# Performance work log

Hardware: AMD Instinct MI355X
Metric: run time of the kernel (lower is better)

The kernel has to match this reference:

```python
import jax, jax.numpy as jnp
import numpy as np

EPS = 1e-5
NEG = -10000.0


def rel_shift(x):
    # x: [B, H, T1, T2] with T2 = 2*T1 - 1 -> returns [B, H, T1, T1]
    B, H, T1, T2 = x.shape
    x = jnp.pad(x, ((0, 0), (0, 0), (0, 0), (1, 0)))        # [B,H,T1,T2+1]
    x = x.reshape(B, H, T2 + 1, T1)[:, :, 1:, :].reshape(B, H, T1, T2)
    return x[:, :, :, : T2 // 2 + 1]


def setup_inputs() -> dict:
    key = jax.random.key(0)
    B, C, T, H = 4, 512, 1024, 8
    ks = jax.random.split(key, 16)
    s = 0.02
    inp = {
        "x": jax.random.normal(ks[0], (B, C, T), jnp.float32),
        "pos_emb": jax.random.normal(ks[1], (1, C, 2 * T - 1), jnp.float32),
        "x_mask": jnp.ones((B, 1, T), jnp.float32),
        "gamma": jnp.ones((C,), jnp.float32),
        "beta": jnp.zeros((C,), jnp.float32),
        "Wq": jax.random.normal(ks[2], (C, C), jnp.float32) * s,
        "bq": jnp.zeros((C,), jnp.float32),
        "Wk": jax.random.normal(ks[3], (C, C), jnp.float32) * s,
        "bk": jnp.zeros((C,), jnp.float32),
        "Wv": jax.random.normal(ks[4], (C, C), jnp.float32) * s,
        "bv": jnp.zeros((C,), jnp.float32),
        "Wp": jax.random.normal(ks[5], (C, C), jnp.float32) * s,
        "u_bias": jax.random.normal(ks[6], (H, C // H), jnp.float32) * s,
        "v_bias": jax.random.normal(ks[7], (H, C // H), jnp.float32) * s,
        "Wo": jax.random.normal(ks[8], (C, C), jnp.float32) * s,
        "bo": jnp.zeros((C,), jnp.float32),
    }
    return inp


def reference(x, pos_emb, x_mask, gamma, beta, Wq, bq, Wk, bk, Wv, bv, Wp,
              u_bias, v_bias, Wo, bo):
    B, C, T = x.shape
    H, Dh = u_bias.shape

    # channel LayerNorm (axis=1)
    mean = jnp.mean(x, axis=1, keepdims=True)
    var = jnp.mean((x - mean) ** 2, axis=1, keepdims=True)
    xn = (x - mean) * jax.lax.rsqrt(var + EPS)
    xn = xn * gamma[None, :, None] + beta[None, :, None]

    conv1x1 = lambda W, b, z: jnp.einsum('oc,bct->bot', W, z) + b[None, :, None]
    q = conv1x1(Wq, bq, xn).reshape(B, H, Dh, T)
    k = conv1x1(Wk, bk, xn).reshape(B, H, Dh, T)
    v = conv1x1(Wv, bv, xn).reshape(B, H, Dh, T)
    p = jnp.einsum('oc,xct->xot', Wp, pos_emb)          # [1, C, 2T-1], no bias
    p = p.reshape(p.shape[0], H, Dh, -1)[0]             # [H, Dh, 2T-1]

    content = jnp.einsum('bhdt,bhds->bhts', q + u_bias[None, :, :, None], k)
    pos = jnp.einsum('bhdt,hds->bhts', q + v_bias[None, :, :, None], p)
    pos = rel_shift(pos)                                 # [B, H, T, T]

    score = (content + pos) / jnp.sqrt(jnp.float32(C))
    attn_mask = x_mask[:, :, None, :] * x_mask[:, :, :, None]  # [B,1,T,T]
    score = jnp.where(attn_mask == 0, NEG, score)
    attn = jax.nn.softmax(score, axis=-1)

    # context[d,t] = sum_s v[d,s] * attn[s,t]
    ctx = jnp.einsum('bhds,bhst->bhdt', v, attn).reshape(B, C, T)
    return jnp.einsum('oc,bct->bot', Wo, ctx) + bo[None, :, None]
```

## Files before the change

### kernel.cpp

```cpp
#include <hip/hip_runtime.h>
#include <hip/hip_bf16.h>
#include <cmath>

typedef unsigned short u16;
typedef __bf16 bf16_t;
typedef bf16_t bf16x8 __attribute__((ext_vector_type(8)));
typedef float f32x4 __attribute__((ext_vector_type(4)));
typedef u16 u16x8 __attribute__((ext_vector_type(8)));

#define MFMA16(A,B,C) __builtin_amdgcn_mfma_f32_16x16x32_bf16(A,B,C,0,0,0)

#define CB 512
#define TT 1024
#define NH 8
#define DH 64
#define ALPHA (0.044194173824159216f * 1.4426950408889634f)
#define MASKL 14426.950408889634f

static __device__ __forceinline__ u16 f2b(float f) {
  unsigned u = __float_as_uint(f);
  unsigned r = u + 0x7FFFu + ((u >> 16) & 1u);
  return (u16)(r >> 16);
}
static __device__ __forceinline__ float b2f(u16 u) {
  return __uint_as_float(((unsigned)u) << 16);
}
static __device__ __forceinline__ bf16x8 ldb8(const u16* p) {
  return *reinterpret_cast<const bf16x8*>(p);
}

__global__ __launch_bounds__(256)
void convert5(const float* __restrict__ Wq, const float* __restrict__ Wk,
              const float* __restrict__ Wv, const float* __restrict__ Wp,
              const float* __restrict__ Wo,
              u16* __restrict__ Wstk, u16* __restrict__ WoB)
{
  int i = blockIdx.x * 256 + threadIdx.x;
  int sel = i >> 15, loc = i & 32767;
  const float* src = (sel == 0) ? Wq : (sel == 1) ? Wk : (sel == 2) ? Wv
                   : (sel == 3) ? Wp : Wo;
  const float4 a = ((const float4*)src)[loc * 2 + 0];
  const float4 b = ((const float4*)src)[loc * 2 + 1];
  u16x8 o;
  o[0] = f2b(a.x); o[1] = f2b(a.y); o[2] = f2b(a.z); o[3] = f2b(a.w);
  o[4] = f2b(b.x); o[5] = f2b(b.y); o[6] = f2b(b.z); o[7] = f2b(b.w);
  u16* dst = (sel < 4) ? (Wstk + (size_t)i * 8) : (WoB + (size_t)loc * 8);
  *(u16x8*)dst = o;
}

__global__ __launch_bounds__(256)
void transpose_pe(const float* __restrict__ pe, u16* __restrict__ posT)
{
  __shared__ float tile[64][65];
  int j0 = blockIdx.x * 64, c0 = blockIdx.y * 64;
  for (int e = threadIdx.x; e < 4096; e += 256) {
    int cc = e >> 6, jj = e & 63;
    int j = j0 + jj;
    tile[jj][cc] = (j < 2047) ? pe[(size_t)(c0 + cc) * 2047 + j] : 0.f;
  }
  __syncthreads();
  for (int e = threadIdx.x; e < 4096; e += 256) {
    int jj = e >> 6, cc = e & 63;
    posT[(size_t)(j0 + jj) * 512 + c0 + cc] = f2b(tile[jj][cc]);
  }
}

__global__ __launch_bounds__(256)
void ln_kernel(const float* __restrict__ x, const float* __restrict__ gamma,
               const float* __restrict__ beta, u16* __restrict__ xnT)
{
  __shared__ float sred[8][33], ssred[8][33];
  int tl = threadIdx.x & 31, cg = threadIdx.x >> 5;
  int t = blockIdx.x * 32 + tl;
  int b = blockIdx.y;
  const float* xb = x + (size_t)b * CB * TT + t;
  float s = 0.f, ss = 0.f;
  for (int c = cg * 64; c < cg * 64 + 64; ++c) {
    float v = xb[(size_t)c * TT];
    s += v; ss += v * v;
  }
  sred[cg][tl] = s; ssred[cg][tl] = ss;
  __syncthreads();
  float S = 0.f, SS = 0.f;
  #pragma unroll
  for (int g = 0; g < 8; ++g) { S += sred[g][tl]; SS += ssred[g][tl]; }
  float mean = S * (1.f / 512.f);
  float var = SS * (1.f / 512.f) - mean * mean;
  float rstd = rsqrtf(var + 1e-5f);
  u16* orow = xnT + ((size_t)b * TT + t) * CB;
  for (int c8 = 0; c8 < 8; ++c8) {
    int c = cg * 64 + c8 * 8;
    u16x8 o;
    #pragma unroll
    for (int j = 0; j < 8; ++j) {
      float v = xb[(size_t)(c + j) * TT];
      o[j] = f2b((v - mean) * rstd * gamma[c + j] + beta[c + j]);
    }
    *(u16x8*)(orow + c) = o;
  }
}

template<int K, int OMODE>
__global__ __launch_bounds__(256)
void gemm2(const u16* __restrict__ A, const u16* __restrict__ XT,
           long xStride, long oStride, int Nout,
           const float* __restrict__ b0, void* __restrict__ outv)
{
  const int tid = threadIdx.x, w = tid >> 6, lane = tid & 63;
  const int ln16 = lane & 15, kg = lane >> 4;
  const int wm = w & 1, wn = w >> 1;
  const int m0 = blockIdx.y * 64 + wm * 32;
  const int n0 = blockIdx.x * 128 + wn * 64;
  const int z = blockIdx.z;
  const u16* Ar = A + (size_t)(m0 + ln16) * K + kg * 8;
  const u16* Br = XT + (size_t)z * xStride + (size_t)(n0 + ln16) * K + kg * 8;
  f32x4 acc[2][4] = {};
  #pragma unroll 2
  for (int ks = 0; ks < K / 32; ++ks) {
    bf16x8 a[2], bb[4];
    #pragma unroll
    for (int mt = 0; mt < 2; ++mt) a[mt] = ldb8(Ar + (size_t)mt * 16 * K + ks * 32);
    #pragma unroll
    for (int nt = 0; nt < 4; ++nt) bb[nt] = ldb8(Br + (size_t)nt * 16 * K + ks * 32);
    #pragma unroll
    for (int mt = 0; mt < 2; ++mt)
      #pragma unroll
      for (int nt = 0; nt < 4; ++nt)
        acc[mt][nt] = MFMA16(a[mt], bb[nt], acc[mt][nt]);
  }
  float add[2][4];
  #pragma unroll
  for (int mt = 0; mt < 2; ++mt)
    #pragma unroll
    for (int jr = 0; jr < 4; ++jr)
      add[mt][jr] = b0 ? b0[m0 + mt * 16 + kg * 4 + jr] : 0.f;
  #pragma unroll
  for (int mt = 0; mt < 2; ++mt)
    #pragma unroll
    for (int nt = 0; nt < 4; ++nt) {
      const int n = n0 + nt * 16 + ln16;
      if constexpr (OMODE == 0) {
        float* out = (float*)outv;
        #pragma unroll
        for (int jr = 0; jr < 4; ++jr)
          out[(size_t)z * oStride + (size_t)(m0 + mt * 16 + kg * 4 + jr) * Nout + n] =
              acc[mt][nt][jr] + add[mt][jr];
      } else {
        const int m_low = m0 + mt * 16;
        const size_t o = (size_t)z * oStride +
                         ((size_t)(m_low >> 6) * Nout + n) * 64 + (m_low & 63) + kg * 4;
        ushort4 s4;
        s4.x = f2b(acc[mt][nt][0] + add[mt][0]);
        s4.y = f2b(acc[mt][nt][1] + add[mt][1]);
        s4.z = f2b(acc[mt][nt][2] + add[mt][2]);
        s4.w = f2b(acc[mt][nt][3] + add[mt][3]);
        *reinterpret_cast<ushort4*>((u16*)outv + o) = s4;
      }
    }
}

__global__ __launch_bounds__(256)
void proj_qkv2(const u16* __restrict__ Wstk, const u16* __restrict__ xnT,
               const float* __restrict__ bq, const float* __restrict__ ub,
               const float* __restrict__ bk, const float* __restrict__ bv,
               u16* __restrict__ quB, u16* __restrict__ kB, u16* __restrict__ vB)
{
  const int tid = threadIdx.x, w = tid >> 6, lane = tid & 63;
  const int ln16 = lane & 15, kg = lane >> 4;
  const int wm = w & 1, wn = w >> 1;
  const int my = blockIdx.y;
  const int sec = my >> 3;
  const int m0l = (my & 7) * 64 + wm * 32;
  const int n0 = blockIdx.x * 128 + wn * 64;
  const int z = blockIdx.z;
  const long XS = (long)TT * CB;
  const long QS = (long)NH * TT * DH;
  const u16* Ar = Wstk + (size_t)(sec * 512 + m0l + ln16) * 512 + kg * 8;
  const u16* Br = xnT + (size_t)z * XS + (size_t)(n0 + ln16) * 512 + kg * 8;
  f32x4 acc[2][4] = {};
  #pragma unroll 2
  for (int ks = 0; ks < 16; ++ks) {
    bf16x8 a[2], bb[4];
    #pragma unroll
    for (int mt = 0; mt < 2; ++mt) a[mt] = ldb8(Ar + (size_t)mt * 16 * 512 + ks * 32);
    #pragma unroll
    for (int nt = 0; nt < 4; ++nt) bb[nt] = ldb8(Br + (size_t)nt * 16 * 512 + ks * 32);
    #pragma unroll
    for (int mt = 0; mt < 2; ++mt)
      #pragma unroll
      for (int nt = 0; nt < 4; ++nt)
        acc[mt][nt] = MFMA16(a[mt], bb[nt], acc[mt][nt]);
  }
  const float scl = (sec == 0) ? ALPHA : 1.f;
  float add[2][4];
  #pragma unroll
  for (int mt = 0; mt < 2; ++mt)
    #pragma unroll
    for (int jr = 0; jr < 4; ++jr) {
      int m = m0l + mt * 16 + kg * 4 + jr;
      add[mt][jr] = (sec == 0) ? (bq[m] + ub[m]) : (sec == 1) ? bk[m] : bv[m];
    }
  if (sec < 2) {
    u16* dst = sec ? kB : quB;
    #pragma unroll
    for (int mt = 0; mt < 2; ++mt)
      #pragma unroll
      for (int nt = 0; nt < 4; ++nt) {
        const int n = n0 + nt * 16 + ln16;
        const int m_low = m0l + mt * 16;
        const size_t o = (size_t)z * QS +
                         ((size_t)(m_low >> 6) * TT + n) * 64 + (m_low & 63) + kg * 4;
        ushort4 s4;
        s4.x = f2b((acc[mt][nt][0] + add[mt][0]) * scl);
        s4.y = f2b((acc[mt][nt][1] + add[mt][1]) * scl);
        s4.z = f2b((acc[mt][nt][2] + add[mt][2]) * scl);
        s4.w = f2b((acc[mt][nt][3] + add[mt][3]) * scl);
        *reinterpret_cast<ushort4*>(dst + o) = s4;
      }
  } else {
    #pragma unroll
    for (int mt = 0; mt < 2; ++mt)
      #pragma unroll
      for (int nt = 0; nt < 4; ++nt) {
        const int n = n0 + nt * 16 + ln16;
        #pragma unroll
        for (int jr = 0; jr < 4; ++jr)
          vB[(size_t)z * QS + (size_t)(m0l + mt * 16 + kg * 4 + jr) * TT + n] =
              f2b(acc[mt][nt][jr] + add[mt][jr]);
      }
  }
}

__global__ __launch_bounds__(256)
void corr_kernel(const u16* __restrict__ pp, const float* __restrict__ ub,
                 const float* __restrict__ vb, float* __restrict__ corr)
{
  const int h = blockIdx.y;
  const int j = blockIdx.x * 256 + threadIdx.x;
  __shared__ float dl[64];
  if (threadIdx.x < 64)
    dl[threadIdx.x] = vb[h * 64 + threadIdx.x] - ub[h * 64 + threadIdx.x];
  __syncthreads();
  const u16* prow = pp + ((size_t)h * 2048 + j) * 64;
  float s = 0.f;
  #pragma unroll
  for (int d8 = 0; d8 < 8; ++d8) {
    union { bf16x8 v; u16 u[8]; } pu;
    pu.v = ldb8(prow + d8 * 8);
    #pragma unroll
    for (int e = 0; e < 8; ++e) s += b2f(pu.u[e]) * dl[d8 * 8 + e];
  }
  corr[h * 2048 + j] = s * ALPHA;
}

__global__ __launch_bounds__(256)
void stats_mfma(const u16* __restrict__ qu, const u16* __restrict__ kk_,
                const u16* __restrict__ pp, const float* __restrict__ corr,
                const float* __restrict__ xmask, float* __restrict__ ls)
{
  const int tid = threadIdx.x;
  const int w = tid >> 6, lane = tid & 63;
  const int ln16 = lane & 15, kg = lane >> 4;
  const int l48 = lane & 48;
  const int bid = blockIdx.x;
  const int bh = (bid & 7) + 8 * ((bid >> 3) & 3);
  const int rest = bid >> 5;
  const int qi0 = (rest & 31) * 32;
  const int part = rest >> 5;
  const int b = bh >> 3, h = bh & 7;
  const u16* quP = qu + (size_t)bh * TT * DH;
  const u16* kP  = kk_ + (size_t)bh * TT * DH;
  const u16* pP  = pp + (size_t)h * 2048 * DH;
  const float* corrP = corr + (h << 11);

  __shared__ float red[4][32];

  bf16x8 qa[2][2];
  #pragma unroll
  for (int mt = 0; mt < 2; ++mt)
    #pragma unroll
    for (int kc = 0; kc < 2; ++kc)
      qa[mt][kc] = ldb8(&quP[(size_t)(qi0 + mt * 16 + ln16) * DH + kc * 32 + kg * 8]);
  float aq[2][4];
  #pragma unroll
  for (int mt = 0; mt < 2; ++mt)
    #pragma unroll
    for (int jr = 0; jr < 4; ++jr)
      aq[mt][jr] = (xmask[b * TT + qi0 + mt * 16 + kg * 4 + jr] - 1.f) * MASKL;

  float rs[2][4] = {};
  for (int c = 0; c < 2; ++c) {
    const int ki0 = (part * 8 + c * 4 + w) * 64;
    const int j0 = ki0 - qi0 + 992;
    #pragma unroll
    for (int mt = 0; mt < 2; ++mt) {
      f32x4 g[6];
      #pragma unroll
      for (int n = 0; n < 6; ++n) {
        const size_t po = (size_t)(j0 + n * 16 + ln16) * DH + kg * 8;
        bf16x8 pb0 = ldb8(&pP[po]);
        bf16x8 pb1 = ldb8(&pP[po + 32]);
        const float cval = corrP[j0 + n * 16 + ln16];
        f32x4 t = {cval, cval, cval, cval};
        t = MFMA16(qa[mt][0], pb0, t);
        t = MFMA16(qa[mt][1], pb1, t);
        g[n] = t;
      }
      f32x4 dd[4];
      #pragma unroll
      for (int nt = 0; nt < 4; ++nt) {
        const size_t ko = (size_t)(ki0 + nt * 16 + ln16) * DH + kg * 8;
        bf16x8 kb0 = ldb8(&kP[ko]);
        bf16x8 kb1 = ldb8(&kP[ko + 32]);
        const float ak = (xmask[b * TT + ki0 + nt * 16 + ln16] - 1.f) * MASKL;
        f32x4 t = { aq[mt][0] + ak, aq[mt][1] + ak, aq[mt][2] + ak, aq[mt][3] + ak };
        t = MFMA16(qa[mt][0], kb0, t);
        t = MFMA16(qa[mt][1], kb1, t);
        dd[nt] = t;
      }
      #pragma unroll
      for (int jr = 0; jr < 4; ++jr) {
        const int qrow = mt * 16 + kg * 4 + jr;
        const int sh = ln16 + 31 - qrow;
        const int src = l48 | (sh & 15);
        const int o = sh >> 4;
        float s[6];
        #pragma unroll
        for (int n = 0; n < 6; ++n) s[n] = __shfl(g[n][jr], src);
        #pragma unroll
        for (int nt = 0; nt < 4; ++nt) {
          const float val = (o == 0) ? s[nt] : (o == 1) ? s[nt + 1] : s[nt + 2];
          rs[mt][jr] += exp2f(dd[nt][jr] + val);
        }
      }
    }
  }
  #pragma unroll
  for (int mt = 0; mt < 2; ++mt)
    #pragma unroll
    for (int jr = 0; jr < 4; ++jr) {
      float v = rs[mt][jr];
      v += __shfl_xor(v, 1); v += __shfl_xor(v, 2);
      v += __shfl_xor(v, 4); v += __shfl_xor(v, 8);
      rs[mt][jr] = v;
    }
  if (ln16 == 0) {
    #pragma unroll
    for (int mt = 0; mt < 2; ++mt)
      #pragma unroll
      for (int jr = 0; jr < 4; ++jr)
        red[w][mt * 16 + kg * 4 + jr] = rs[mt][jr];
  }
  __syncthreads();
  if (tid < 32)
    ls[(size_t)part * 32768 + (size_t)bh * TT + qi0 + tid] =
        red[0][tid] + red[1][tid] + red[2][tid] + red[3][tid];
}

__global__ __launch_bounds__(256)
void ctx_mfma(const u16* __restrict__ qu, const u16* __restrict__ kk_,
              const u16* __restrict__ vv, const u16* __restrict__ pp,
              const float* __restrict__ corr, const float* __restrict__ xmask,
              u16* __restrict__ ctx2)
{
  const int tid = threadIdx.x;
  const int w = tid >> 6, lane = tid & 63;
  const int ln16 = lane & 15, kg = lane >> 4;
  const int l48 = lane & 48;
  const int bid = blockIdx.x;
  const int bh = (bid & 7) + 8 * ((bid >> 3) & 3);
  const int rest = bid >> 5;
  const int t0 = (rest & 15) * 64;
  const int part = rest >> 4;
  const int b = bh >> 3, h = bh & 7;
  const u16* quP = qu + (size_t)bh * TT * DH;
  const u16* kP  = kk_ + (size_t)bh * TT * DH;
  const u16* vP  = vv + (size_t)bh * DH * TT;
  const u16* pP  = pp + (size_t)h * 2048 * DH;
  const float* corrP = corr + (h << 11);

  __shared__ __align__(16) u16 P[2][64][72];

  bf16x8 ka[4][2];
  #pragma unroll
  for (int nt = 0; nt < 4; ++nt)
    #pragma unroll
    for (int kc = 0; kc < 2; ++kc)
      ka[nt][kc] = ldb8(&kP[(size_t)(t0 + nt * 16 + ln16) * DH + kc * 32 + kg * 8]);
  float at4[4];
  #pragma unroll
  for (int nt = 0; nt < 4; ++nt)
    at4[nt] = (xmask[b * TT + t0 + nt * 16 + ln16] - 1.f) * MASKL;

  auto scores = [&](int qcn, int buf) {
    const int qw = qcn * 64 + w * 16;
    const int j0 = t0 - qw + 1008;
    const size_t qo = (size_t)(qw + ln16) * DH + kg * 8;
    bf16x8 qa0 = ldb8(&quP[qo]), qa1 = ldb8(&quP[qo + 32]);
    f32x4 g[5];
    #pragma unroll
    for (int n = 0; n < 5; ++n) {
      const size_t po = (size_t)(j0 + n * 16 + ln16) * DH + kg * 8;
      bf16x8 pb0 = ldb8(&pP[po]), pb1 = ldb8(&pP[po + 32]);
      const float cval = corrP[j0 + n * 16 + ln16];
      f32x4 t = {cval, cval, cval, cval};
      t = MFMA16(qa0, pb0, t);
      t = MFMA16(qa1, pb1, t);
      g[n] = t;
    }
    float sg[4][5];
    #pragma unroll
    for (int jr = 0; jr < 4; ++jr) {
      const int qrow = kg * 4 + jr;
      const int src = l48 | ((ln16 + 15 - qrow) & 15);
      #pragma unroll
      for (int n = 0; n < 5; ++n) sg[jr][n] = __shfl(g[n][jr], src);
    }
    float aqv[4];
    #pragma unroll
    for (int jr = 0; jr < 4; ++jr)
      aqv[jr] = (xmask[b * TT + qw + kg * 4 + jr] - 1.f) * MASKL;
    #pragma unroll
    for (int nt = 0; nt < 4; ++nt) {
      f32x4 dd = { aqv[0] + at4[nt], aqv[1] + at4[nt],
                   aqv[2] + at4[nt], aqv[3] + at4[nt] };
      dd = MFMA16(qa0, ka[nt][0], dd);
      dd = MFMA16(qa1, ka[nt][1], dd);
      unsigned lo = 0, hi = 0;
      #pragma unroll
      for (int jr = 0; jr < 4; ++jr) {
        const int qrow = kg * 4 + jr;
        const float val = (ln16 <= qrow) ? sg[jr][nt] : sg[jr][nt + 1];
        const float e = exp2f(dd[jr] + val);
        const unsigned bb = f2b(e);
        if (jr == 0) lo = bb; else if (jr == 1) lo |= bb << 16;
        else if (jr == 2) hi = bb; else hi |= bb << 16;
      }
      *reinterpret_cast<uint2*>(&P[buf][nt * 16 + ln16][w * 16 + kg * 4]) =
          make_uint2(lo, hi);
    }
  };

  f32x4 cacc[4] = {};
  scores(part * 4, 0);
  __syncthreads();
  #pragma unroll
  for (int i = 0; i < 4; ++i) {
    const int qc = part * 4 + i;
    const size_t vbase = (size_t)(w * 16 + ln16) * TT + qc * 64 + kg * 8;
    bf16x8 vf0 = ldb8(&vP[vbase]), vf1 = ldb8(&vP[vbase + 32]);
    #pragma unroll
    for (int nt = 0; nt < 4; ++nt) {
      bf16x8 pb0 = *reinterpret_cast<const bf16x8*>(&P[i & 1][nt * 16 + ln16][kg * 8]);
      bf16x8 pb1 = *reinterpret_cast<const bf16x8*>(&P[i & 1][nt * 16 + ln16][32 + kg * 8]);
      cacc[nt] = MFMA16(vf0, pb0, cacc[nt]);
      cacc[nt] = MFMA16(vf1, pb1, cacc[nt]);
    }
    if (i < 3) {
      scores(qc + 1, (i + 1) & 1);
      __syncthreads();
    }
  }
  #pragma unroll
  for (int nt = 0; nt < 4; ++nt) {
    const int t = t0 + nt * 16 + ln16;
    ushort4 s4;
    s4.x = f2b(cacc[nt][0]); s4.y = f2b(cacc[nt][1]);
    s4.z = f2b(cacc[nt][2]); s4.w = f2b(cacc[nt][3]);
    *reinterpret_cast<ushort4*>(
      &ctx2[((size_t)b * TT + t) * 2048 + part * 512 + h * 64 + w * 16 + kg * 4]) = s4;
  }
}

__global__ __launch_bounds__(256)
void vscale(u16* __restrict__ vv, const float* __restrict__ ls)
{
  int i = blockIdx.x * 256 + threadIdx.x;
  int bh = i >> 13;
  int rem = i & 8191;
  int d = rem >> 7;
  int qi0 = (rem & 127) * 8;
  const float* lsP = ls + bh * 1024 + qi0;
  u16* row = vv + ((size_t)bh * 64 + d) * 1024 + qi0;
  union { u16x8 v; u16 u[8]; } t;
  t.v = *(u16x8*)row;
  u16x8 o;
  #pragma unroll
  for (int e = 0; e < 8; ++e) {
    float linv = __builtin_amdgcn_rcpf(lsP[e] + lsP[32768 + e]);
    o[e] = f2b(b2f(t.u[e]) * linv);
  }
  *(u16x8*)row = o;
}

__global__ __launch_bounds__(256)
void reduce_ctx(const u16* __restrict__ ctx2, u16* __restrict__ ctxS)
{
  int i = blockIdx.x * 256 + threadIdx.x;
  int row = i >> 6;
  int c0 = (i & 63) * 8;
  const u16* src = ctx2 + (size_t)row * 2048 + c0;
  float s[8] = {};
  #pragma unroll
  for (int p = 0; p < 4; ++p) {
    union { u16x8 v; u16 u[8]; } t;
    t.v = *(const u16x8*)(src + p * 512);
    #pragma unroll
    for (int e = 0; e < 8; ++e) s[e] += b2f(t.u[e]);
  }
  u16x8 o;
  #pragma unroll
  for (int e = 0; e < 8; ++e) o[e] = f2b(s[e]);
  *(u16x8*)(ctxS + (size_t)row * 512 + c0) = o;
}

extern "C" void kernel_launch(void* const* d_in, const int* in_sizes, int n_in,
                              void* d_out, int out_size, void* d_ws, size_t ws_size,
                              hipStream_t stream)
{
  (void)in_sizes; (void)n_in; (void)out_size;
  const float* x     = (const float*)d_in[0];
  const float* pe    = (const float*)d_in[1];
  const float* xm    = (const float*)d_in[2];
  const float* gamma = (const float*)d_in[3];
  const float* beta  = (const float*)d_in[4];
  const float* Wq    = (const float*)d_in[5];
  const float* bq    = (const float*)d_in[6];
  const float* Wk    = (const float*)d_in[7];
  const float* bk    = (const float*)d_in[8];
  const float* Wv    = (const float*)d_in[9];
  const float* bv    = (const float*)d_in[10];
  const float* Wp    = (const float*)d_in[11];
  const float* ub    = (const float*)d_in[12];
  const float* vb    = (const float*)d_in[13];
  const float* Wo    = (const float*)d_in[14];
  const float* bo    = (const float*)d_in[15];

  char* ws = (char*)d_ws;
  u16*  quB  = (u16*) (ws + 0);
  u16*  ctxS = (u16*) (ws + 0);
  u16*  kB   = (u16*) (ws + 4194304);
  u16*  vB   = (u16*) (ws + 8388608);
  u16*  pB   = (u16*) (ws + 12582912);
  float* corrB = (float*)(ws + 14680064);
  float* lsB = (float*)(ws + 14745600);
  u16*  WoB  = (u16*) (ws + 15007744);
  u16*  ctx2 = (u16*) (ws + 15532032);
  u16*  xnT  = (u16*) (ws + 15532032);
  u16*  posT = (u16*) (ws + 19726336);
  u16*  Wstk = (u16*) (ws + 21823488);
  if (ws_size < 32309248) return;

  dim3 blk(256);

  convert5<<<dim3(640), blk, 0, stream>>>(Wq, Wk, Wv, Wp, Wo, Wstk, WoB);
  transpose_pe<<<dim3(32, 8), blk, 0, stream>>>(pe, posT);
  ln_kernel<<<dim3(32, 4), blk, 0, stream>>>(x, gamma, beta, xnT);

  proj_qkv2<<<dim3(8, 24, 4), blk, 0, stream>>>(Wstk, xnT, bq, ub, bk, bv, quB, kB, vB);
  gemm2<512, 1><<<dim3(16, 8, 1), blk, 0, stream>>>(
      Wstk + (size_t)1536 * 512, posT, 0, 0, 2048, nullptr, pB);
  corr_kernel<<<dim3(8, 8), blk, 0, stream>>>(pB, ub, vb, corrB);

  stats_mfma<<<dim3(2048), blk, 0, stream>>>(quB, kB, pB, corrB, xm, lsB);
  vscale<<<dim3(1024), blk, 0, stream>>>(vB, lsB);
  ctx_mfma<<<dim3(2048), blk, 0, stream>>>(quB, kB, vB, pB, corrB, xm, ctx2);
  reduce_ctx<<<dim3(1024), blk, 0, stream>>>(ctx2, ctxS);

  gemm2<512, 0><<<dim3(8, 8, 4), blk, 0, stream>>>(
      WoB, ctxS, (long)TT * CB, (long)CB * TT, TT, bo, (float*)d_out);
}
```

Measured before the change: 233.9 us.

## Stage positional scores in LDS for rel-shift and add smaller-tile output GEMM

In the stats kernel, the relative-shift gather no longer uses per-element cross-lane shuffles with a three-way select. The positional score tiles are now written as bf16 into a per-wave shared-memory buffer and read back at the shifted index. This removes many shuffles but adds LDS traffic and an extra bf16 rounding of the positional term. Separately, the output projection switches to a dedicated GEMM with 64x64 tiles, launching more blocks to raise occupancy.

```diff
diff --git a/kernel.cpp b/kernel.cpp
--- a/kernel.cpp
+++ b/kernel.cpp
@@ -160,6 +160,48 @@
 }
 
 __global__ __launch_bounds__(256)
+void gemm3_out(const u16* __restrict__ A, const u16* __restrict__ XT,
+               const float* __restrict__ b0, float* __restrict__ out)
+{
+  const int tid = threadIdx.x, w = tid >> 6, lane = tid & 63;
+  const int ln16 = lane & 15, kg = lane >> 4;
+  const int m0 = blockIdx.y * 64 + (w & 1) * 32;
+  const int n0 = blockIdx.x * 64 + (w >> 1) * 32;
+  const int z = blockIdx.z;
+  const u16* Ar = A + (size_t)(m0 + ln16) * 512 + kg * 8;
+  const u16* Br = XT + (size_t)z * (512 * 1024) + (size_t)(n0 + ln16) * 512 + kg * 8;
+  f32x4 acc[2][2] = {};
+  #pragma unroll 2
+  for (int ks = 0; ks < 16; ++ks) {
+    bf16x8 a[2], bb[2];
+    #pragma unroll
+    for (int mt = 0; mt < 2; ++mt) a[mt] = ldb8(Ar + (size_t)mt * 16 * 512 + ks * 32);
+    #pragma unroll
+    for (int nt = 0; nt < 2; ++nt) bb[nt] = ldb8(Br + (size_t)nt * 16 * 512 + ks * 32);
+    #pragma unroll
+    for (int mt = 0; mt < 2; ++mt)
+      #pragma unroll
+      for (int nt = 0; nt < 2; ++nt)
+        acc[mt][nt] = MFMA16(a[mt], bb[nt], acc[mt][nt]);
+  }
+  #pragma unroll
+  for (int mt = 0; mt < 2; ++mt) {
+    float add[4];
+    #pragma unroll
+    for (int jr = 0; jr < 4; ++jr)
+      add[jr] = b0[m0 + mt * 16 + kg * 4 + jr];
+    #pragma unroll
+    for (int nt = 0; nt < 2; ++nt) {
+      const int n = n0 + nt * 16 + ln16;
+      #pragma unroll
+      for (int jr = 0; jr < 4; ++jr)
+        out[(size_t)z * (512 * 1024) + (size_t)(m0 + mt * 16 + kg * 4 + jr) * 1024 + n] =
+            acc[mt][nt][jr] + add[jr];
+    }
+  }
+}
+
+__global__ __launch_bounds__(256)
 void proj_qkv2(const u16* __restrict__ Wstk, const u16* __restrict__ xnT,
                const float* __restrict__ bq, const float* __restrict__ ub,
                const float* __restrict__ bk, const float* __restrict__ bv,
@@ -261,7 +303,6 @@
   const int tid = threadIdx.x;
   const int w = tid >> 6, lane = tid & 63;
   const int ln16 = lane & 15, kg = lane >> 4;
-  const int l48 = lane & 48;
   const int bid = blockIdx.x;
   const int bh = (bid & 7) + 8 * ((bid >> 3) & 3);
   const int rest = bid >> 5;
@@ -273,6 +314,7 @@
   const u16* pP  = pp + (size_t)h * 2048 * DH;
   const float* corrP = corr + (h << 11);
 
+  __shared__ u16 G[4][32][100];
   __shared__ float red[4][32];
 
   bf16x8 qa[2][2];
@@ -293,44 +335,37 @@
     const int ki0 = (part * 8 + c * 4 + w) * 64;
     const int j0 = ki0 - qi0 + 992;
     #pragma unroll
-    for (int mt = 0; mt < 2; ++mt) {
-      f32x4 g[6];
-      #pragma unroll
-      for (int n = 0; n < 6; ++n) {
-        const size_t po = (size_t)(j0 + n * 16 + ln16) * DH + kg * 8;
-        bf16x8 pb0 = ldb8(&pP[po]);
-        bf16x8 pb1 = ldb8(&pP[po + 32]);
-        const float cval = corrP[j0 + n * 16 + ln16];
-        f32x4 t = {cval, cval, cval, cval};
-        t = MFMA16(qa[mt][0], pb0, t);
-        t = MFMA16(qa[mt][1], pb1, t);
-        g[n] = t;
+    for (int nt = 0; nt < 6; ++nt) {
+      const size_t po = (size_t)(j0 + nt * 16 + ln16) * DH + kg * 8;
+      bf16x8 pb0 = ldb8(&pP[po]);
+      bf16x8 pb1 = ldb8(&pP[po + 32]);
+      const float cval = corrP[j0 + nt * 16 + ln16];
+      #pragma unroll
+      for (int mt = 0; mt < 2; ++mt) {
+        f32x4 g = {0.f, 0.f, 0.f, 0.f};
+        g = MFMA16(qa[mt][0], pb0, g);
+        g = MFMA16(qa[mt][1], pb1, g);
+        #pragma unroll
+        for (int jr = 0; jr < 4; ++jr)
+          G[w][mt * 16 + kg * 4 + jr][nt * 16 + ln16] = f2b(g[jr] + cval);
       }
-      f32x4 dd[4];
-      #pragma unroll
-      for (int nt = 0; nt < 4; ++nt) {
-        const size_t ko = (size_t)(ki0 + nt * 16 + ln16) * DH + kg * 8;
-        bf16x8 kb0 = ldb8(&kP[ko]);
-        bf16x8 kb1 = ldb8(&kP[ko + 32]);
-        const float ak = (xmask[b * TT + ki0 + nt * 16 + ln16] - 1.f) * MASKL;
-        f32x4 t = { aq[mt][0] + ak, aq[mt][1] + ak, aq[mt][2] + ak, aq[mt][3] + ak };
-        t = MFMA16(qa[mt][0], kb0, t);
-        t = MFMA16(qa[mt][1], kb1, t);
-        dd[nt] = t;
-      }
-      #pragma unroll
-      for (int jr = 0; jr < 4; ++jr) {
-        const int qrow = mt * 16 + kg * 4 + jr;
-        const int sh = ln16 + 31 - qrow;
-        const int src = l48 | (sh & 15);
-        const int o = sh >> 4;
-        float s[6];
+    }
+    #pragma unroll
+    for (int nt = 0; nt < 4; ++nt) {
+      const size_t ko = (size_t)(ki0 + nt * 16 + ln16) * DH + kg * 8;
+      bf16x8 kb0 = ldb8(&kP[ko]);
+      bf16x8 kb1 = ldb8(&kP[ko + 32]);
+      const float ak = (xmask[b * TT + ki0 + nt * 16 + ln16] - 1.f) * MASKL;
+      #pragma unroll
+      for (int mt = 0; mt < 2; ++mt) {
+        f32x4 dd = { aq[mt][0] + ak, aq[mt][1] + ak, aq[mt][2] + ak, aq[mt][3] + ak };
+        dd = MFMA16(qa[mt][0], kb0, dd);
+        dd = MFMA16(qa[mt][1], kb1, dd);
         #pragma unroll
-        for (int n = 0; n < 6; ++n) s[n] = __shfl(g[n][jr], src);
-        #pragma unroll
-        for (int nt = 0; nt < 4; ++nt) {
-          const float val = (o == 0) ? s[nt] : (o == 1) ? s[nt + 1] : s[nt + 2];
-          rs[mt][jr] += exp2f(dd[nt][jr] + val);
+        for (int jr = 0; jr < 4; ++jr) {
+          const int qrow = mt * 16 + kg * 4 + jr;
+          const int u = nt * 16 + ln16 - qrow + 31;
+          rs[mt][jr] += exp2f(dd[jr] + b2f(G[w][qrow][u]));
         }
       }
     }
@@ -567,6 +602,5 @@
   ctx_mfma<<<dim3(2048), blk, 0, stream>>>(quB, kB, vB, pB, corrB, xm, ctx2);
   reduce_ctx<<<dim3(1024), blk, 0, stream>>>(ctx2, ctxS);
 
-  gemm2<512, 0><<<dim3(8, 8, 4), blk, 0, stream>>>(
-      WoB, ctxS, (long)TT * CB, (long)CB * TT, TT, bo, (float*)d_out);
-}
+  gemm3_out<<<dim3(16, 8, 4), blk, 0, stream>>>(WoB, ctxS, bo, (float*)d_out);
+}
```

Measured after the change: 214.3 us. -8.4%, faster.
